# Performance work log

Measured on AMD Instinct MI355X. Metric: run time of the kernel, lower is better.

The kernel has to match this reference:

```python
import jax, jax.numpy as jnp
import numpy as np

B, S, D, R, N = 4, 2048, 1024, 256, 16

def setup_inputs() -> dict:
    key = jax.random.key(0)
    k1, k2, k3, k4, k5 = jax.random.split(key, 5)
    return {
        "x": jax.random.normal(k1, (B, S, D), dtype=jnp.float32),
        "feature_know": jax.random.normal(k2, (N, D, R), dtype=jnp.float32) * 0.02,
        "restore_know": jax.random.normal(k3, (N, R, D), dtype=jnp.float32) * 0.02,
        "feature_know_w": jax.random.uniform(k4, (B, S, N), dtype=jnp.float32),
        "restore_know_w": jax.random.uniform(k5, (B, S, N), dtype=jnp.float32),
    }

def reference(x, feature_know, restore_know, feature_know_w, restore_know_w):
    # Feature stage: weighted mixture over N knowledge neurons, D -> R.
    # Same math as einsum('bsd,ndr->bsnr') then einsum('bsnr,bsn->bsr'),
    # fused so the [B,S,N,R] intermediate is reduced over N on the fly.
    h = jnp.einsum('bsd,ndr,bsn->bsr', x, feature_know, feature_know_w)
    # Restore stage: R -> D, again a weighted mixture over N neurons.
    out = jnp.einsum('bsr,nrd,bsn->bsd', h, restore_know, restore_know_w)
    # Dropout is evaluated deterministically (eval mode): identity.
    return out
```

## Files before the change

kernel.cpp:

```cpp
#include <hip/hip_runtime.h>

typedef unsigned short u16;
typedef unsigned int u32;
typedef __attribute__((ext_vector_type(4))) float f32x4;
typedef __attribute__((ext_vector_type(8))) short bf16x8;
typedef __attribute__((ext_vector_type(4))) unsigned short u16x4;

#define MFMA(a, b, c) __builtin_amdgcn_mfma_f32_16x16x32_bf16((a), (b), (c), 0, 0, 0)

static constexpr int M_TOK = 8192;

__device__ __forceinline__ u16 f2bf(float f) {
  u32 u = __float_as_uint(f);
  return (u16)((u + 0x7FFFu + ((u >> 16) & 1u)) >> 16);
}
__device__ __forceinline__ float bf2f(u16 b) {
  u32 u = ((u32)b) << 16;
  return __uint_as_float(u);
}
__device__ __forceinline__ void gload16(const u16* g, u16* l) {
  __builtin_amdgcn_global_load_lds(
      (const __attribute__((address_space(1))) u32*)(const void*)g,
      (__attribute__((address_space(3))) u32*)(void*)l, 16, 0, 0);
}

#define PH_BAR()                                     \
  do {                                               \
    __builtin_amdgcn_sched_barrier(0);               \
    __builtin_amdgcn_s_barrier();                    \
    asm volatile("s_waitcnt lgkmcnt(0)" ::: "memory"); \
    __builtin_amdgcn_sched_barrier(0);               \
  } while (0)
#define PH_END()                       \
  do {                                 \
    __builtin_amdgcn_sched_barrier(0); \
    __builtin_amdgcn_s_barrier();      \
  } while (0)

__global__ void cast_x_kernel(const float* __restrict__ in, u16* __restrict__ out, int total4) {
  for (int i = blockIdx.x * blockDim.x + threadIdx.x; i < total4; i += gridDim.x * blockDim.x) {
    float4 v = ((const float4*)in)[i];
    u16x4 o;
    o[0] = f2bf(v.x); o[1] = f2bf(v.y); o[2] = f2bf(v.z); o[3] = f2bf(v.w);
    ((u16x4*)out)[i] = o;
  }
}

__global__ void tcast_kernel(const float* __restrict__ in, u16* __restrict__ out, int P, int Q) {
  __shared__ float tile[32][33];
  const int z = blockIdx.z;
  const int q0 = blockIdx.x * 32, p0 = blockIdx.y * 32;
  const float* src = in + (size_t)z * P * Q;
  u16* dst = out + (size_t)z * P * Q;
  const int tx = threadIdx.x & 31, ty = threadIdx.x >> 5;
#pragma unroll
  for (int k = 0; k < 4; ++k)
    tile[ty + k * 8][tx] = src[(size_t)(p0 + ty + k * 8) * Q + q0 + tx];
  __syncthreads();
#pragma unroll
  for (int k = 0; k < 4; ++k)
    dst[(size_t)(q0 + ty + k * 8) * P + p0 + tx] = f2bf(tile[tx][ty + k * 8]);
}

__global__ void combine_h(const u16* __restrict__ T, const float* __restrict__ Wf,
                          u16* __restrict__ h) {
  const int m = blockIdx.x * 4 + (threadIdx.x >> 6);
  const int lane = threadIdx.x & 63;
  const u16* rowp = T + (size_t)m * 4096;
  float h0 = 0.f, h1 = 0.f, h2 = 0.f, h3 = 0.f;
#pragma unroll
  for (int n = 0; n < 16; ++n) {
    u16x4 v = *(const u16x4*)&rowp[n * 256 + lane * 4];
    const float wf = Wf[(size_t)m * 16 + n];
    h0 += wf * bf2f(v[0]); h1 += wf * bf2f(v[1]);
    h2 += wf * bf2f(v[2]); h3 += wf * bf2f(v[3]);
  }
  u16x4 o;
  o[0] = f2bf(h0); o[1] = f2bf(h1); o[2] = f2bf(h2); o[3] = f2bf(h3);
  *(u16x4*)&h[(size_t)m * 256 + lane * 4] = o;
}

template <int NT>
__global__ __launch_bounds__(512, 2) void gemm256(
    const u16* __restrict__ A, const u16* __restrict__ Bm, void* __restrict__ OutV,
    const int N, const int K) {
  constexpr int NITER = NT / 2;
  __shared__ u16 ldsA[2][2][8192];
  __shared__ u16 ldsB[2][2][8192];

  const int tid = threadIdx.x;
  const int lane = tid & 63;
  const int wid = tid >> 6;
  const int wr = wid >> 2, wc = wid & 3;

  const int nwg = gridDim.x * gridDim.y;
  int wgid = blockIdx.y * gridDim.x + blockIdx.x;
  wgid = (wgid & 7) * (nwg >> 3) + (wgid >> 3);
  const int by = wgid / gridDim.x, bx = wgid - by * gridDim.x;
  const int m0 = by * 256, bn0 = bx * 256;

  const int arow = lane & 15;
  const int acol = (lane >> 4) * 16;
  const int sw = (arow & 7) << 4;
  const int lo0 = arow * 128 + (acol ^ sw);
  const int lo1 = arow * 128 + ((64 + acol) ^ sw);

  const u16* Abase = A + (size_t)m0 * K;
  const u16* Bbase = Bm + (size_t)bn0 * K;

  f32x4 acc[8][4];
#pragma unroll
  for (int i = 0; i < 8; ++i)
#pragma unroll
    for (int j = 0; j < 4; ++j) acc[i][j] = (f32x4){0.f, 0.f, 0.f, 0.f};

  auto STAGE = [&](int b, int isB, int hf, int kt) {
    const u16* G = isB ? Bbase : Abase;
    u16* L = isB ? &ldsB[b][hf][0] : &ldsA[b][hf][0];
#pragma unroll
    for (int j = 0; j < 2; ++j) {
      const int q = j * 8192 + tid * 16;
      const int grow = q >> 7;
      const int gcol = ((q & 127) ^ (((q >> 7) & 7) << 4)) >> 1;
      gload16(G + (size_t)(hf * 128 + grow) * K + kt * 64 + gcol,
              L + ((j * 8192 + wid * 1024) >> 1));
    }
  };
  auto LOAD_AV = [&](bf16x8 (&v)[4][2], int b, int mh) {
    const char* p = (const char*)&ldsA[b][0][0] + (wr * 128 + mh * 64) * 128;
#pragma unroll
    for (int mi = 0; mi < 4; ++mi) {
      v[mi][0] = *(const bf16x8*)(p + mi * 2048 + lo0);
      v[mi][1] = *(const bf16x8*)(p + mi * 2048 + lo1);
    }
  };
  auto LOAD_BV = [&](bf16x8 (&v)[2][2], int b, int nq) {
#pragma unroll
    for (int nj = 0; nj < 2; ++nj) {
      const int rb = wc * 64 + (nq * 2 + nj) * 16;
      const char* p = (const char*)&ldsB[b][0][0] + rb * 128;
      v[nj][0] = *(const bf16x8*)(p + lo0);
      v[nj][1] = *(const bf16x8*)(p + lo1);
    }
  };

#define QUAD(AV, BV, MH, NQ)                                                   \
  do {                                                                         \
    _Pragma("unroll") for (int mi = 0; mi < 4; ++mi) {                         \
      _Pragma("unroll") for (int nj = 0; nj < 2; ++nj) {                       \
        acc[(MH)*4 + mi][(NQ)*2 + nj] =                                        \
            MFMA(AV[mi][0], BV[nj][0], acc[(MH)*4 + mi][(NQ)*2 + nj]);         \
        acc[(MH)*4 + mi][(NQ)*2 + nj] =                                        \
            MFMA(AV[mi][1], BV[nj][1], acc[(MH)*4 + mi][(NQ)*2 + nj]);         \
      }                                                                        \
    }                                                                          \
  } while (0)

  bf16x8 av[4][2], avh[4][2], bv0[2][2], bv1[2][2];

  STAGE(0, 0, 0, 0); STAGE(0, 0, 1, 0); STAGE(0, 1, 0, 0); STAGE(0, 1, 1, 0);
  STAGE(1, 1, 0, 1); STAGE(1, 0, 0, 1);
  asm volatile("s_waitcnt vmcnt(4)" ::: "memory");
  __builtin_amdgcn_sched_barrier(0);
  __builtin_amdgcn_s_barrier();

#pragma unroll 1
  for (int i = 0; i < NITER; ++i) {
    const int ta = 2 * i, tb = ta + 1;
    const bool st = (i + 1 < NITER);
    LOAD_AV(av, 0, 0); LOAD_BV(bv0, 0, 0); STAGE(1, 0, 1, tb);
    PH_BAR();
    __builtin_amdgcn_s_setprio(1); QUAD(av, bv0, 0, 0); __builtin_amdgcn_s_setprio(0);
    PH_END();
    LOAD_BV(bv1, 0, 1); STAGE(1, 1, 1, tb);
    PH_BAR();
    __builtin_amdgcn_s_setprio(1); QUAD(av, bv1, 0, 1); __builtin_amdgcn_s_setprio(0);
    PH_END();
    LOAD_AV(avh, 0, 1); if (st) STAGE(0, 1, 0, ta + 2);
    PH_BAR();
    __builtin_amdgcn_s_setprio(1); QUAD(avh, bv0, 1, 0); __builtin_amdgcn_s_setprio(0);
    PH_END();
    if (st) STAGE(0, 0, 0, ta + 2);
    PH_BAR();
    __builtin_amdgcn_s_setprio(1); QUAD(avh, bv1, 1, 1); __builtin_amdgcn_s_setprio(0);
    if (st) asm volatile("s_waitcnt vmcnt(4)" ::: "memory");
    else    asm volatile("s_waitcnt vmcnt(0)" ::: "memory");
    PH_END();
    LOAD_AV(av, 1, 0); LOAD_BV(bv0, 1, 0); if (st) STAGE(0, 0, 1, ta + 2);
    PH_BAR();
    __builtin_amdgcn_s_setprio(1); QUAD(av, bv0, 0, 0); __builtin_amdgcn_s_setprio(0);
    PH_END();
    LOAD_BV(bv1, 1, 1); if (st) STAGE(0, 1, 1, ta + 2);
    PH_BAR();
    __builtin_amdgcn_s_setprio(1); QUAD(av, bv1, 0, 1); __builtin_amdgcn_s_setprio(0);
    PH_END();
    LOAD_AV(avh, 1, 1); if (st) STAGE(1, 1, 0, tb + 2);
    PH_BAR();
    __builtin_amdgcn_s_setprio(1); QUAD(avh, bv0, 1, 0); __builtin_amdgcn_s_setprio(0);
    PH_END();
    if (st) STAGE(1, 0, 0, tb + 2);
    PH_BAR();
    __builtin_amdgcn_s_setprio(1); QUAD(avh, bv1, 1, 1); __builtin_amdgcn_s_setprio(0);
    if (st) asm volatile("s_waitcnt vmcnt(4)" ::: "memory");
    PH_END();
  }

#pragma unroll
  for (int MI = 0; MI < 8; ++MI) {
    const int row = m0 + wr * 128 + MI * 16 + (lane >> 4) * 4;
#pragma unroll
    for (int NJ = 0; NJ < 4; ++NJ) {
      const int col = bn0 + wc * 64 + NJ * 16 + (lane & 15);
      u16* p = (u16*)OutV + (size_t)row * N + col;
#pragma unroll
      for (int j = 0; j < 4; ++j) p[(size_t)j * N] = f2bf(acc[MI][NJ][j]);
    }
  }
}
#undef QUAD

__global__ __launch_bounds__(512, 2) void gemm_fold(
    const u16* __restrict__ A,
    const u16* __restrict__ Bn,
    const float* __restrict__ W,
    float* __restrict__ Out) {
  __shared__ u16 ldsB[8][8192];
  __shared__ u16 Wlds[16][264];

  const int tid = threadIdx.x;
  const int lane = tid & 63;
  const int wid = tid >> 6;
  const int kh = wid >> 2;
  const int wrM = (wid >> 1) & 1;
  const int wcN = wid & 1;

  const int nwg = gridDim.x * gridDim.y;
  int wgid = blockIdx.y * gridDim.x + blockIdx.x;
  wgid = (wgid & 7) * (nwg >> 3) + (wgid >> 3);
  const int by = wgid / gridDim.x, bx = wgid - by * gridDim.x;
  const int m0 = by * 128, d0 = bx * 128;

  const int arow = lane & 15;
  const int acol = (lane >> 4) * 16;
  const int sw = (arow & 7) << 4;
  const int lo0 = arow * 128 + (acol ^ sw);
  const int lo1 = arow * 128 + ((64 + acol) ^ sw);

  for (int i = tid; i < 128 * 16; i += 512) {
    const int row = i >> 4, n = i & 15;
    Wlds[n][row] = f2bf(W[(size_t)(m0 + row) * 16 + n]);
  }

  auto ASTAGE = [&](int kt) {
    const u16* G = A + (size_t)m0 * 256;
    u16* L = &ldsB[kt][0];
#pragma unroll
    for (int j = 0; j < 2; ++j) {
      const int q = j * 8192 + tid * 16;
      const int grow = q >> 7;
      const int gcol = ((q & 127) ^ (((q >> 7) & 7) << 4)) >> 1;
      gload16(G + (size_t)grow * 256 + kt * 64 + gcol, L + ((j * 8192 + wid * 1024) >> 1));
    }
  };
  ASTAGE(0); ASTAGE(1); ASTAGE(2); ASTAGE(3);
  __syncthreads();
  bf16x8 avk[4][4];
#pragma unroll
  for (int c2 = 0; c2 < 2; ++c2) {
#pragma unroll
    for (int mi = 0; mi < 4; ++mi) {
      const char* p = (const char*)&ldsB[kh * 2 + c2][0] + (wrM * 64 + mi * 16) * 128;
      avk[c2 * 2 + 0][mi] = *(const bf16x8*)(p + lo0);
      avk[c2 * 2 + 1][mi] = *(const bf16x8*)(p + lo1);
    }
  }
  __syncthreads();

  auto BSTAGE = [&](int ss) {
    const int n = ss >> 1, h = ss & 1, p = ss & 3;
    const u16* G = Bn + ((size_t)n * 1024 + d0) * 256;
#pragma unroll
    for (int t = 0; t < 2; ++t) {
      u16* L = &ldsB[2 * p + t][0];
      const int kt = h + 2 * t;
#pragma unroll
      for (int j = 0; j < 2; ++j) {
        const int q = j * 8192 + tid * 16;
        const int grow = q >> 7;
        const int gcol = ((q & 127) ^ (((q >> 7) & 7) << 4)) >> 1;
        gload16(G + (size_t)grow * 256 + kt * 64 + gcol, L + ((j * 8192 + wid * 1024) >> 1));
      }
    }
  };

  f32x4 acc_t[4][4], acc_g[4][4];
#pragma unroll
  for (int mi = 0; mi < 4; ++mi)
#pragma unroll
    for (int nj = 0; nj < 4; ++nj) {
      acc_t[mi][nj] = (f32x4){0.f, 0.f, 0.f, 0.f};
      acc_g[mi][nj] = (f32x4){0.f, 0.f, 0.f, 0.f};
    }
  bf16x8 bv[4][2];

  BSTAGE(0); BSTAGE(1); BSTAGE(2);
  asm volatile("s_waitcnt vmcnt(8)" ::: "memory");
  __builtin_amdgcn_sched_barrier(0);
  __builtin_amdgcn_s_barrier();

  auto SSTEP = [&](int ss, int h, bool do_stage, int vmsel) {
    const int p = ss & 3;
    const char* pB = (const char*)&ldsB[2 * p + kh][0];
#pragma unroll
    for (int nj = 0; nj < 4; ++nj) {
      const char* q = pB + (wcN * 64 + nj * 16) * 128;
      bv[nj][0] = *(const bf16x8*)(q + lo0);
      bv[nj][1] = *(const bf16x8*)(q + lo1);
    }
    if (do_stage) BSTAGE(ss + 3);
    PH_BAR();
    __builtin_amdgcn_s_setprio(1);
#pragma unroll
    for (int mi = 0; mi < 4; ++mi)
#pragma unroll
      for (int nj = 0; nj < 4; ++nj) {
        acc_g[mi][nj] = MFMA(avk[2 * h + 0][mi], bv[nj][0], acc_g[mi][nj]);
        acc_g[mi][nj] = MFMA(avk[2 * h + 1][mi], bv[nj][1], acc_g[mi][nj]);
      }
    __builtin_amdgcn_s_setprio(0);
    if (vmsel == 8)      asm volatile("s_waitcnt vmcnt(8)" ::: "memory");
    else if (vmsel == 4) asm volatile("s_waitcnt vmcnt(4)" ::: "memory");
    else if (vmsel == 0) asm volatile("s_waitcnt vmcnt(0)" ::: "memory");
    PH_END();
  };
  auto FOLD = [&](int n) {
#pragma unroll
    for (int mi = 0; mi < 4; ++mi) {
      const int rbase = wrM * 64 + mi * 16 + (lane >> 4) * 4;
      u16x4 wq = *(const u16x4*)&Wlds[n][rbase];
      const float w0 = bf2f(wq[0]), w1 = bf2f(wq[1]), w2 = bf2f(wq[2]), w3 = bf2f(wq[3]);
#pragma unroll
      for (int nj = 0; nj < 4; ++nj) {
        acc_t[mi][nj][0] += w0 * acc_g[mi][nj][0];
        acc_t[mi][nj][1] += w1 * acc_g[mi][nj][1];
        acc_t[mi][nj][2] += w2 * acc_g[mi][nj][2];
        acc_t[mi][nj][3] += w3 * acc_g[mi][nj][3];
        acc_g[mi][nj] = (f32x4){0.f, 0.f, 0.f, 0.f};
      }
    }
  };

#pragma unroll 1
  for (int nn = 0; nn < 14; ++nn) {
    SSTEP(nn * 2 + 0, 0, true, 8);
    SSTEP(nn * 2 + 1, 1, true, 8);
    FOLD(nn);
  }
  SSTEP(28, 0, true, 8);
  SSTEP(29, 1, false, 4);
  FOLD(14);
  SSTEP(30, 0, false, 0);
  SSTEP(31, 1, false, -1);
  FOLD(15);

  __syncthreads();
  float* red = (float*)&ldsB[0][0];
  const int reg = (wrM * 2 + wcN) * 4096;
  if (kh == 1) {
#pragma unroll
    for (int mi = 0; mi < 4; ++mi)
#pragma unroll
      for (int j = 0; j < 4; ++j) {
        const int r = mi * 16 + (lane >> 4) * 4 + j;
#pragma unroll
        for (int nj = 0; nj < 4; ++nj)
          red[reg + r * 64 + nj * 16 + (lane & 15)] = acc_t[mi][nj][j];
      }
  }
  __syncthreads();
  if (kh == 0) {
#pragma unroll
    for (int mi = 0; mi < 4; ++mi) {
      const int rr = mi * 16 + (lane >> 4) * 4;
#pragma unroll
      for (int j = 0; j < 4; ++j) {
        float* orow = Out + (size_t)(m0 + wrM * 64 + rr + j) * 1024 + d0 + wcN * 64 + (lane & 15);
#pragma unroll
        for (int nj = 0; nj < 4; ++nj)
          orow[nj * 16] = acc_t[mi][nj][j] + red[reg + (rr + j) * 64 + nj * 16 + (lane & 15)];
      }
    }
  }
}

extern "C" void kernel_launch(void* const* d_in, const int* in_sizes, int n_in,
                              void* d_out, int out_size, void* d_ws, size_t ws_size,
                              hipStream_t stream) {
  const float* x  = (const float*)d_in[0];
  const float* F  = (const float*)d_in[1];
  const float* Rk = (const float*)d_in[2];
  const float* Wf = (const float*)d_in[3];
  const float* Wr = (const float*)d_in[4];
  float* out = (float*)d_out;

  char* ws = (char*)d_ws;
  u16* X16 = (u16*)(ws);
  u16* B1  = (u16*)(ws + (16u << 20));
  u16* Rt  = (u16*)(ws + (24u << 20));
  u16* T   = (u16*)(ws + (32u << 20));
  u16* h16 = (u16*)(ws);

  cast_x_kernel<<<2048, 256, 0, stream>>>(x, X16, (M_TOK * 1024) / 4);
  tcast_kernel<<<dim3(8, 32, 16), 256, 0, stream>>>(F, B1, 1024, 256);
  tcast_kernel<<<dim3(32, 8, 16), 256, 0, stream>>>(Rk, Rt, 256, 1024);

  gemm256<16><<<dim3(16, 32, 1), 512, 0, stream>>>(X16, B1, T, 4096, 1024);

  combine_h<<<2048, 256, 0, stream>>>(T, Wf, h16);

  gemm_fold<<<dim3(8, 64, 1), 512, 0, stream>>>(h16, Rt, Wr, out);
}
```

Before: 180.9 us.

## Remap workgroups to per-XCD tile windows and merge pipeline phases

Both GEMM kernels replace the simple XCD round-robin remap with a mapping that gives each chiplet a compact 2D window of output tiles (4x8 for gemm256, 2x16 for gemm_fold), so tiles sharing A and B rows land on the same L2. The gemm256 main loop also merges pairs of phases: it loads both B fragments up front, issues two stage loads per phase and runs two QUAD blocks per barrier, halving the barrier count. The merged phases raise register pressure and issue global loads in larger bursts, which may hurt overlap. The window mapping hardcodes the grid sizes (64 groups per XCD).

```diff
diff --git a/kernel.cpp b/kernel.cpp
--- a/kernel.cpp
+++ b/kernel.cpp
@@ -93,10 +93,13 @@
   const int wid = tid >> 6;
   const int wr = wid >> 2, wc = wid & 3;
 
-  const int nwg = gridDim.x * gridDim.y;
-  int wgid = blockIdx.y * gridDim.x + blockIdx.x;
-  wgid = (wgid & 7) * (nwg >> 3) + (wgid >> 3);
-  const int by = wgid / gridDim.x, bx = wgid - by * gridDim.x;
+  {
+  }
+  const int L = blockIdx.y * gridDim.x + blockIdx.x;
+  const int ordered = (L & 7) * 64 + (L >> 3);
+  const int cid = ordered >> 5, win = ordered & 31;
+  const int bx = (cid & 3) * 4 + (win & 3);
+  const int by = (cid >> 2) * 8 + (win >> 2);
   const int m0 = by * 256, bn0 = bx * 256;
 
   const int arow = lane & 15;
@@ -116,14 +119,14 @@
 
   auto STAGE = [&](int b, int isB, int hf, int kt) {
     const u16* G = isB ? Bbase : Abase;
-    u16* L = isB ? &ldsB[b][hf][0] : &ldsA[b][hf][0];
+    u16* L2p = isB ? &ldsB[b][hf][0] : &ldsA[b][hf][0];
 #pragma unroll
     for (int j = 0; j < 2; ++j) {
       const int q = j * 8192 + tid * 16;
       const int grow = q >> 7;
       const int gcol = ((q & 127) ^ (((q >> 7) & 7) << 4)) >> 1;
       gload16(G + (size_t)(hf * 128 + grow) * K + kt * 64 + gcol,
-              L + ((j * 8192 + wid * 1024) >> 1));
+              L2p + ((j * 8192 + wid * 1024) >> 1));
     }
   };
   auto LOAD_AV = [&](bf16x8 (&v)[4][2], int b, int mh) {
@@ -168,39 +171,35 @@
   for (int i = 0; i < NITER; ++i) {
     const int ta = 2 * i, tb = ta + 1;
     const bool st = (i + 1 < NITER);
-    LOAD_AV(av, 0, 0); LOAD_BV(bv0, 0, 0); STAGE(1, 0, 1, tb);
+    LOAD_AV(av, 0, 0); LOAD_BV(bv0, 0, 0); LOAD_BV(bv1, 0, 1);
+    STAGE(1, 0, 1, tb); STAGE(1, 1, 1, tb);
     PH_BAR();
-    __builtin_amdgcn_s_setprio(1); QUAD(av, bv0, 0, 0); __builtin_amdgcn_s_setprio(0);
+    __builtin_amdgcn_s_setprio(1);
+    QUAD(av, bv0, 0, 0); QUAD(av, bv1, 0, 1);
+    __builtin_amdgcn_s_setprio(0);
     PH_END();
-    LOAD_BV(bv1, 0, 1); STAGE(1, 1, 1, tb);
+    LOAD_AV(avh, 0, 1);
+    if (st) { STAGE(0, 1, 0, ta + 2); STAGE(0, 0, 0, ta + 2); }
     PH_BAR();
-    __builtin_amdgcn_s_setprio(1); QUAD(av, bv1, 0, 1); __builtin_amdgcn_s_setprio(0);
-    PH_END();
-    LOAD_AV(avh, 0, 1); if (st) STAGE(0, 1, 0, ta + 2);
-    PH_BAR();
-    __builtin_amdgcn_s_setprio(1); QUAD(avh, bv0, 1, 0); __builtin_amdgcn_s_setprio(0);
-    PH_END();
-    if (st) STAGE(0, 0, 0, ta + 2);
-    PH_BAR();
-    __builtin_amdgcn_s_setprio(1); QUAD(avh, bv1, 1, 1); __builtin_amdgcn_s_setprio(0);
+    __builtin_amdgcn_s_setprio(1);
+    QUAD(avh, bv0, 1, 0); QUAD(avh, bv1, 1, 1);
+    __builtin_amdgcn_s_setprio(0);
     if (st) asm volatile("s_waitcnt vmcnt(4)" ::: "memory");
     else    asm volatile("s_waitcnt vmcnt(0)" ::: "memory");
     PH_END();
-    LOAD_AV(av, 1, 0); LOAD_BV(bv0, 1, 0); if (st) STAGE(0, 0, 1, ta + 2);
+    LOAD_AV(av, 1, 0); LOAD_BV(bv0, 1, 0); LOAD_BV(bv1, 1, 1);
+    if (st) { STAGE(0, 0, 1, ta + 2); STAGE(0, 1, 1, ta + 2); }
     PH_BAR();
-    __builtin_amdgcn_s_setprio(1); QUAD(av, bv0, 0, 0); __builtin_amdgcn_s_setprio(0);
+    __builtin_amdgcn_s_setprio(1);
+    QUAD(av, bv0, 0, 0); QUAD(av, bv1, 0, 1);
+    __builtin_amdgcn_s_setprio(0);
     PH_END();
-    LOAD_BV(bv1, 1, 1); if (st) STAGE(0, 1, 1, ta + 2);
+    LOAD_AV(avh, 1, 1);
+    if (st) { STAGE(1, 1, 0, tb + 2); STAGE(1, 0, 0, tb + 2); }
     PH_BAR();
-    __builtin_amdgcn_s_setprio(1); QUAD(av, bv1, 0, 1); __builtin_amdgcn_s_setprio(0);
-    PH_END();
-    LOAD_AV(avh, 1, 1); if (st) STAGE(1, 1, 0, tb + 2);
-    PH_BAR();
-    __builtin_amdgcn_s_setprio(1); QUAD(avh, bv0, 1, 0); __builtin_amdgcn_s_setprio(0);
-    PH_END();
-    if (st) STAGE(1, 0, 0, tb + 2);
-    PH_BAR();
-    __builtin_amdgcn_s_setprio(1); QUAD(avh, bv1, 1, 1); __builtin_amdgcn_s_setprio(0);
+    __builtin_amdgcn_s_setprio(1);
+    QUAD(avh, bv0, 1, 0); QUAD(avh, bv1, 1, 1);
+    __builtin_amdgcn_s_setprio(0);
     if (st) asm volatile("s_waitcnt vmcnt(4)" ::: "memory");
     PH_END();
   }
@@ -234,10 +233,11 @@
   const int wrM = (wid >> 1) & 1;
   const int wcN = wid & 1;
 
-  const int nwg = gridDim.x * gridDim.y;
-  int wgid = blockIdx.y * gridDim.x + blockIdx.x;
-  wgid = (wgid & 7) * (nwg >> 3) + (wgid >> 3);
-  const int by = wgid / gridDim.x, bx = wgid - by * gridDim.x;
+  const int L = blockIdx.y * gridDim.x + blockIdx.x;
+  const int ordered = (L & 7) * 64 + (L >> 3);
+  const int cid = ordered >> 5, win = ordered & 31;
+  const int bx = (cid & 3) * 2 + (win & 1);
+  const int by = (cid >> 2) * 16 + (win >> 1);
   const int m0 = by * 128, d0 = bx * 128;
 
   const int arow = lane & 15;
@@ -253,13 +253,13 @@
 
   auto ASTAGE = [&](int kt) {
     const u16* G = A + (size_t)m0 * 256;
-    u16* L = &ldsB[kt][0];
+    u16* Lp = &ldsB[kt][0];
 #pragma unroll
     for (int j = 0; j < 2; ++j) {
       const int q = j * 8192 + tid * 16;
       const int grow = q >> 7;
       const int gcol = ((q & 127) ^ (((q >> 7) & 7) << 4)) >> 1;
-      gload16(G + (size_t)grow * 256 + kt * 64 + gcol, L + ((j * 8192 + wid * 1024) >> 1));
+      gload16(G + (size_t)grow * 256 + kt * 64 + gcol, Lp + ((j * 8192 + wid * 1024) >> 1));
     }
   };
   ASTAGE(0); ASTAGE(1); ASTAGE(2); ASTAGE(3);
@@ -281,14 +281,14 @@
     const u16* G = Bn + ((size_t)n * 1024 + d0) * 256;
 #pragma unroll
     for (int t = 0; t < 2; ++t) {
-      u16* L = &ldsB[2 * p + t][0];
+      u16* Lp = &ldsB[2 * p + t][0];
       const int kt = h + 2 * t;
 #pragma unroll
       for (int j = 0; j < 2; ++j) {
         const int q = j * 8192 + tid * 16;
         const int grow = q >> 7;
         const int gcol = ((q & 127) ^ (((q >> 7) & 7) << 4)) >> 1;
-        gload16(G + (size_t)grow * 256 + kt * 64 + gcol, L + ((j * 8192 + wid * 1024) >> 1));
+        gload16(G + (size_t)grow * 256 + kt * 64 + gcol, Lp + ((j * 8192 + wid * 1024) >> 1));
       }
     }
   };
@@ -415,8 +415,6 @@
   tcast_kernel<<<dim3(32, 8, 16), 256, 0, stream>>>(Rk, Rt, 256, 1024);
 
   gemm256<16><<<dim3(16, 32, 1), 512, 0, stream>>>(X16, B1, T, 4096, 1024);
-
   combine_h<<<2048, 256, 0, stream>>>(T, Wf, h16);
-
   gemm_fold<<<dim3(8, 64, 1), 512, 0, stream>>>(h16, Rt, Wr, out);
 }
```

New measurement: 171.0 us. 5.5% less time.
